# Optimization experiments

Hardware: AMD Instinct MI355X
Metric: run time of the kernel (lower is better)

## Reference

```python
import jax, jax.numpy as jnp
import numpy as np

B = 65536
L, R, D, C = 4, 8, 16, 4
M = D * C          # 64 = d_s2*C
D_S1C = 32         # d_s1*C
OUT = 8


def setup_inputs() -> dict:
    key = jax.random.key(0)
    ks = jax.random.split(key, 16)
    inp = {
        'x': jax.random.uniform(ks[0], (B, 8), dtype=jnp.float32),
        'H': jax.random.normal(ks[1], (B, L, R, D, C), dtype=jnp.float32) * 0.1,
        # VNNILinear / Linear params (not quantized by default -> plain F.linear)
        'W_bit': jax.random.normal(ks[2], (D_S1C, 8), dtype=jnp.float32) * 0.02,
        'b_bit': jnp.zeros((D_S1C,), jnp.float32),
        'W_bridge': jax.random.normal(ks[3], (M, D_S1C), dtype=jnp.float32) * 0.02,
        'W_read': jax.random.normal(ks[4], (OUT, R * M), dtype=jnp.float32) * 0.02,
        'b_read': jnp.zeros((OUT,), jnp.float32),
        # Governor
        'W_sh': jax.random.normal(ks[5], (64, M), dtype=jnp.float32) * 0.02,
        'b_sh': jnp.zeros((64,), jnp.float32),
        'W_eng': jax.random.normal(ks[6], (1, 64), dtype=jnp.float32) * 0.02,
        'b_eng': jnp.zeros((1,), jnp.float32),
        'W_imp': jax.random.normal(ks[7], (1, 64), dtype=jnp.float32) * 0.02,
        'b_imp': jnp.zeros((1,), jnp.float32),
        # surprise heads
        'W_sur': jax.random.normal(ks[8], (1, D_S1C), dtype=jnp.float32) * 0.02,
        'b_sur': jnp.zeros((1,), jnp.float32),
        'W_gate': jax.random.normal(ks[9], (1, D_S1C), dtype=jnp.float32) * 0.02,
        'b_gate': jnp.zeros((1,), jnp.float32),
        # stacked per-slot params
        'decays': jnp.zeros((L, R, M), jnp.float32),
        'halt_w': jax.random.normal(ks[10], (L, R, M), dtype=jnp.float32) * 0.01,
        'halt_b': jnp.zeros((L,), jnp.float32),
    }
    return inp


def reference(x, H, W_bit, b_bit, W_bridge, W_read, b_read, W_sh, b_sh,
              W_eng, b_eng, W_imp, b_imp, W_sur, b_sur, W_gate, b_gate,
              decays, halt_w, halt_b):
    # bit -> s1 latent
    s1 = x @ W_bit.T + b_bit                                   # [B, 32]
    surprise = (jax.nn.sigmoid(s1 @ W_sur.T + b_sur) *
                jax.nn.sigmoid(s1 @ W_gate.T + b_gate))        # [B, 1]
    # bridge to working space
    s2 = jnp.tanh(s1 @ W_bridge.T)                             # [B, 64]
    # governor gates
    hg = jax.nn.relu(s2 @ W_sh.T + b_sh)                       # [B, 64]
    eng = jax.nn.sigmoid(hg @ W_eng.T + b_eng)                 # [B, 1]
    imp = jax.nn.sigmoid(hg @ W_imp.T + b_imp)                 # [B, 1]
    # per-(L,R)-slot halting gate
    halt = jax.nn.sigmoid(jnp.einsum('bm,lrm->blr', s2, halt_w)
                          + halt_b[:, None])                   # [B, L, R]
    gate = halt * (eng * imp)[:, :, None]                      # [B, L, R]
    # gated decay + write into memory slab
    decay_g = jax.nn.sigmoid(decays)                           # [L, R, M]
    Hf = H.reshape(H.shape[0], L, R, M)                        # [B, L, R, M]
    write = (surprise * s2)[:, None, None, :]                  # [B, 1, 1, M]
    H_new = Hf * decay_g[None] + gate[..., None] * write       # [B, L, R, M]
    # read: mean over layers, flatten slots, quantizable readout
    read = H_new.mean(axis=1).reshape(H.shape[0], R * M)       # [B, 512]
    out = read @ W_read.T + b_read                             # [B, 8]
    return out
```

## Files before the change

kernel.cpp:

```cpp
#include <hip/hip_runtime.h>

__device__ __forceinline__ float sigf(float v) {
    return 1.0f / (1.0f + __expf(-v));
}
__device__ __forceinline__ float tanh_fast(float v) {
    return 1.0f - 2.0f / (__expf(2.0f * v) + 1.0f);
}

__global__ __launch_bounds__(256, 1)
void organism_fused(const float* __restrict__ x,
                    const float* __restrict__ H,
                    const float* __restrict__ W_bit,
                    const float* __restrict__ b_bit,
                    const float* __restrict__ W_bridge,
                    const float* __restrict__ W_read,
                    const float* __restrict__ b_read,
                    const float* __restrict__ W_sh,
                    const float* __restrict__ b_sh,
                    const float* __restrict__ W_eng,
                    const float* __restrict__ b_eng,
                    const float* __restrict__ W_imp,
                    const float* __restrict__ b_imp,
                    const float* __restrict__ W_sur,
                    const float* __restrict__ b_sur,
                    const float* __restrict__ W_gate,
                    const float* __restrict__ b_gate,
                    const float* __restrict__ decays,
                    const float* __restrict__ halt_w,
                    const float* __restrict__ halt_b,
                    float* __restrict__ out)
{
    const int b = blockIdx.x * 256 + threadIdx.x;

    float xv[8];
    {
        const float4 x0 = *(const float4*)(x + (size_t)b * 8);
        const float4 x1 = *(const float4*)(x + (size_t)b * 8 + 4);
        xv[0]=x0.x; xv[1]=x0.y; xv[2]=x0.z; xv[3]=x0.w;
        xv[4]=x1.x; xv[5]=x1.y; xv[6]=x1.z; xv[7]=x1.w;
    }

    float s1[32];
#pragma unroll
    for (int i = 0; i < 32; ++i) {
        float a = b_bit[i];
#pragma unroll
        for (int k = 0; k < 8; ++k) a += W_bit[i*8+k] * xv[k];
        s1[i] = a;
    }

    float sa = b_sur[0], ga = b_gate[0];
#pragma unroll
    for (int i = 0; i < 32; ++i) {
        sa += W_sur[i]  * s1[i];
        ga += W_gate[i] * s1[i];
    }
    const float sur = sigf(sa) * sigf(ga);

    float s2[64];
#pragma unroll
    for (int m = 0; m < 64; ++m) {
        float a = 0.0f;
#pragma unroll
        for (int i = 0; i < 32; ++i) a += W_bridge[m*32+i] * s1[i];
        s2[m] = tanh_fast(a);
    }

    float ea = b_eng[0], ia = b_imp[0];
    for (int n = 0; n < 64; ++n) {
        float a = b_sh[n];
#pragma unroll
        for (int m = 0; m < 64; ++m) a += W_sh[n*64+m] * s2[m];
        a = fmaxf(a, 0.0f);
        ea += W_eng[n] * a;
        ia += W_imp[n] * a;
    }
    const float ei = sigf(ea) * sigf(ia);

    float wv[64];
#pragma unroll
    for (int m = 0; m < 64; ++m) wv[m] = sur * s2[m];

    float out2[8] = {0,0,0,0,0,0,0,0};
    for (int r = 0; r < 8; ++r) {
        float hs = 0.0f;
#pragma unroll
        for (int l = 0; l < 4; ++l) {
            float a = halt_b[l];
#pragma unroll
            for (int m = 0; m < 64; ++m) a += halt_w[(l*8+r)*64+m] * s2[m];
            hs += sigf(a);
        }
        const float gr = 0.25f * ei * hs;
#pragma unroll
        for (int o = 0; o < 8; ++o) {
            float p = 0.0f;
#pragma unroll
            for (int m = 0; m < 64; ++m) p += W_read[o*512 + r*64 + m] * wv[m];
            out2[o] += gr * p;
        }
    }

    const float* __restrict__ Hrow = H + (size_t)b * 2048;
    float acc[8] = {0,0,0,0,0,0,0,0};

    const int wid = blockIdx.x * 4 + (threadIdx.x >> 6);
    const int rot = (wid & 7) << 6;

    float4 hA[4][2], hB[4][2];

    auto loadblk = [&](float4 (&h)[4][2], int ib) {
        const int rmb = ((ib << 3) + rot) & 511;
#pragma unroll
        for (int l = 0; l < 4; ++l) {
            h[l][0] = *(const float4*)(Hrow + l*512 + rmb);
            h[l][1] = *(const float4*)(Hrow + l*512 + rmb + 4);
        }
    };
    auto compute = [&](const float4 (&h)[4][2], int ib) {
        const int rmb = ((ib << 3) + rot) & 511;
        float s[8] = {0,0,0,0,0,0,0,0};
#pragma unroll
        for (int l = 0; l < 4; ++l) {
#pragma unroll
            for (int q = 0; q < 2; ++q) {
                const float4 d = *(const float4*)(decays + l*512 + rmb + q*4);
                const float4 hh = h[l][q];
                s[q*4+0] += sigf(d.x) * hh.x;
                s[q*4+1] += sigf(d.y) * hh.y;
                s[q*4+2] += sigf(d.z) * hh.z;
                s[q*4+3] += sigf(d.w) * hh.w;
            }
        }
#pragma unroll
        for (int c = 0; c < 8; ++c) s[c] *= 0.25f;
#pragma unroll
        for (int o = 0; o < 8; ++o) {
#pragma unroll
            for (int q = 0; q < 2; ++q) {
                const float4 wr = *(const float4*)(W_read + o*512 + rmb + q*4);
                acc[o] += wr.x*s[q*4+0] + wr.y*s[q*4+1]
                        + wr.z*s[q*4+2] + wr.w*s[q*4+3];
            }
        }
    };

    loadblk(hA, 0);
#pragma unroll 1
    for (int p = 0; p < 32; ++p) {
        loadblk(hB, 2*p + 1);
        compute(hA, 2*p);
        if (p + 1 < 32) loadblk(hA, 2*p + 2);
        compute(hB, 2*p + 1);
    }

    float4 r0, r1;
    r0.x = acc[0] + out2[0] + b_read[0];
    r0.y = acc[1] + out2[1] + b_read[1];
    r0.z = acc[2] + out2[2] + b_read[2];
    r0.w = acc[3] + out2[3] + b_read[3];
    r1.x = acc[4] + out2[4] + b_read[4];
    r1.y = acc[5] + out2[5] + b_read[5];
    r1.z = acc[6] + out2[6] + b_read[6];
    r1.w = acc[7] + out2[7] + b_read[7];
    *(float4*)(out + (size_t)b * 8)     = r0;
    *(float4*)(out + (size_t)b * 8 + 4) = r1;
}

extern "C" void kernel_launch(void* const* d_in, const int* in_sizes, int n_in,
                              void* d_out, int out_size, void* d_ws, size_t ws_size,
                              hipStream_t stream) {
    (void)n_in; (void)d_ws; (void)ws_size; (void)out_size;
    const float* x        = (const float*)d_in[0];
    const float* H        = (const float*)d_in[1];
    const float* W_bit    = (const float*)d_in[2];
    const float* b_bit    = (const float*)d_in[3];
    const float* W_bridge = (const float*)d_in[4];
    const float* W_read   = (const float*)d_in[5];
    const float* b_read   = (const float*)d_in[6];
    const float* W_sh     = (const float*)d_in[7];
    const float* b_sh     = (const float*)d_in[8];
    const float* W_eng    = (const float*)d_in[9];
    const float* b_eng    = (const float*)d_in[10];
    const float* W_imp    = (const float*)d_in[11];
    const float* b_imp    = (const float*)d_in[12];
    const float* W_sur    = (const float*)d_in[13];
    const float* b_sur    = (const float*)d_in[14];
    const float* W_gate   = (const float*)d_in[15];
    const float* b_gate   = (const float*)d_in[16];
    const float* decays   = (const float*)d_in[17];
    const float* halt_w   = (const float*)d_in[18];
    const float* halt_b   = (const float*)d_in[19];
    float* out = (float*)d_out;

    const int B = in_sizes[1] / 2048;
    dim3 grid(B / 256), block(256);
    hipLaunchKernelGGL(organism_fused, grid, block, 0, stream,
                       x, H, W_bit, b_bit, W_bridge, W_read, b_read,
                       W_sh, b_sh, W_eng, b_eng, W_imp, b_imp,
                       W_sur, b_sur, W_gate, b_gate, decays, halt_w, halt_b,
                       out);
}
```

Measured before the change: 975.8 us.

## Precompute decay sigmoids and stage H through an LDS transpose for coalesced loads

A small prep kernel computes 0.25*sigmoid(decays) once into workspace. This removes the per-row recomputation of 2048 sigmoids in every thread. The main kernel now runs one wavefront per block. That wave loads the H rows of its 64 batch rows cooperatively with coalesced float4 loads and transposes them through a double-buffered, padded LDS tile, prefetching the next chunk into registers. The cost is about 35KB of LDS per single-wave block, which limits occupancy. The code also relies on wave-lockstep LDS ordering instead of explicit barriers.

```diff
diff --git a/kernel.cpp b/kernel.cpp
--- a/kernel.cpp
+++ b/kernel.cpp
@@ -7,35 +7,53 @@
     return 1.0f - 2.0f / (__expf(2.0f * v) + 1.0f);
 }
 
-__global__ __launch_bounds__(256, 1)
-void organism_fused(const float* __restrict__ x,
-                    const float* __restrict__ H,
-                    const float* __restrict__ W_bit,
-                    const float* __restrict__ b_bit,
-                    const float* __restrict__ W_bridge,
-                    const float* __restrict__ W_read,
-                    const float* __restrict__ b_read,
-                    const float* __restrict__ W_sh,
-                    const float* __restrict__ b_sh,
-                    const float* __restrict__ W_eng,
-                    const float* __restrict__ b_eng,
-                    const float* __restrict__ W_imp,
-                    const float* __restrict__ b_imp,
-                    const float* __restrict__ W_sur,
-                    const float* __restrict__ b_sur,
-                    const float* __restrict__ W_gate,
-                    const float* __restrict__ b_gate,
-                    const float* __restrict__ decays,
-                    const float* __restrict__ halt_w,
-                    const float* __restrict__ halt_b,
-                    float* __restrict__ out)
+__global__ void organism_prep(const float* __restrict__ decays,
+                              float* __restrict__ sigd4) {
+    const int i = blockIdx.x * 256 + threadIdx.x;
+    if (i < 2048) sigd4[i] = 0.25f * sigf(decays[i]);
+}
+
+__global__ __launch_bounds__(64)
+void organism_main(const float* __restrict__ x,
+                   const float* __restrict__ H,
+                   const float* __restrict__ W_bit,
+                   const float* __restrict__ b_bit,
+                   const float* __restrict__ W_bridge,
+                   const float* __restrict__ W_read,
+                   const float* __restrict__ b_read,
+                   const float* __restrict__ W_sh,
+                   const float* __restrict__ b_sh,
+                   const float* __restrict__ W_eng,
+                   const float* __restrict__ b_eng,
+                   const float* __restrict__ W_imp,
+                   const float* __restrict__ b_imp,
+                   const float* __restrict__ W_sur,
+                   const float* __restrict__ b_sur,
+                   const float* __restrict__ W_gate,
+                   const float* __restrict__ b_gate,
+                   const float* __restrict__ halt_w,
+                   const float* __restrict__ halt_b,
+                   const float* __restrict__ sigd4,
+                   float* __restrict__ out)
 {
-    const int b = blockIdx.x * 256 + threadIdx.x;
+    const int t   = threadIdx.x;
+    const int row = blockIdx.x * 64 + t;
+    const int lr  = t >> 4;
+    const int lj  = t & 15;
+
+    __shared__ float tile[2][64 * 68];
+
+    const float* __restrict__ Hblk = H + (size_t)blockIdx.x * 64 * 2048;
+
+    float4 pf[16];
+#pragma unroll
+    for (int i = 0; i < 16; ++i)
+        pf[i] = *(const float4*)(Hblk + (size_t)(4 * i + lr) * 2048 + lj * 4);
 
     float xv[8];
     {
-        const float4 x0 = *(const float4*)(x + (size_t)b * 8);
-        const float4 x1 = *(const float4*)(x + (size_t)b * 8 + 4);
+        const float4 x0 = *(const float4*)(x + (size_t)row * 8);
+        const float4 x1 = *(const float4*)(x + (size_t)row * 8 + 4);
         xv[0]=x0.x; xv[1]=x0.y; xv[2]=x0.z; xv[3]=x0.w;
         xv[4]=x1.x; xv[5]=x1.y; xv[6]=x1.z; xv[7]=x1.w;
     }
@@ -101,57 +119,60 @@
         }
     }
 
-    const float* __restrict__ Hrow = H + (size_t)b * 2048;
     float acc[8] = {0,0,0,0,0,0,0,0};
-
-    const int wid = blockIdx.x * 4 + (threadIdx.x >> 6);
-    const int rot = (wid & 7) << 6;
-
-    float4 hA[4][2], hB[4][2];
-
-    auto loadblk = [&](float4 (&h)[4][2], int ib) {
-        const int rmb = ((ib << 3) + rot) & 511;
+    float g[64];
+    int buf = 0;
+
+    auto store_tile = [&](int b) {
+#pragma unroll
+        for (int i = 0; i < 16; ++i)
+            *(float4*)(&tile[b][(4 * i + lr) * 68 + lj * 4]) = pf[i];
+    };
+    auto prefetch = [&](int c, int l) {
+#pragma unroll
+        for (int i = 0; i < 16; ++i)
+            pf[i] = *(const float4*)(Hblk + (size_t)(4 * i + lr) * 2048
+                                     + l * 512 + c * 64 + lj * 4);
+    };
+
+#pragma unroll 1
+    for (int c = 0; c < 8; ++c) {
 #pragma unroll
         for (int l = 0; l < 4; ++l) {
-            h[l][0] = *(const float4*)(Hrow + l*512 + rmb);
-            h[l][1] = *(const float4*)(Hrow + l*512 + rmb + 4);
-        }
-    };
-    auto compute = [&](const float4 (&h)[4][2], int ib) {
-        const int rmb = ((ib << 3) + rot) & 511;
-        float s[8] = {0,0,0,0,0,0,0,0};
-#pragma unroll
-        for (int l = 0; l < 4; ++l) {
-#pragma unroll
-            for (int q = 0; q < 2; ++q) {
-                const float4 d = *(const float4*)(decays + l*512 + rmb + q*4);
-                const float4 hh = h[l][q];
-                s[q*4+0] += sigf(d.x) * hh.x;
-                s[q*4+1] += sigf(d.y) * hh.y;
-                s[q*4+2] += sigf(d.z) * hh.z;
-                s[q*4+3] += sigf(d.w) * hh.w;
+            store_tile(buf);
+            if (l < 3)           prefetch(c, l + 1);
+            else if (c < 7)      prefetch(c + 1, 0);
+            const float* __restrict__ tr = &tile[buf][t * 68];
+            const float* __restrict__ sd = sigd4 + l * 512 + c * 64;
+            if (l == 0) {
+#pragma unroll
+                for (int j = 0; j < 64; j += 4) {
+                    const float4 h = *(const float4*)(tr + j);
+                    g[j]   = sd[j]   * h.x;
+                    g[j+1] = sd[j+1] * h.y;
+                    g[j+2] = sd[j+2] * h.z;
+                    g[j+3] = sd[j+3] * h.w;
+                }
+            } else {
+#pragma unroll
+                for (int j = 0; j < 64; j += 4) {
+                    const float4 h = *(const float4*)(tr + j);
+                    g[j]   += sd[j]   * h.x;
+                    g[j+1] += sd[j+1] * h.y;
+                    g[j+2] += sd[j+2] * h.z;
+                    g[j+3] += sd[j+3] * h.w;
+                }
             }
-        }
-#pragma unroll
-        for (int c = 0; c < 8; ++c) s[c] *= 0.25f;
+            buf ^= 1;
+        }
 #pragma unroll
         for (int o = 0; o < 8; ++o) {
-#pragma unroll
-            for (int q = 0; q < 2; ++q) {
-                const float4 wr = *(const float4*)(W_read + o*512 + rmb + q*4);
-                acc[o] += wr.x*s[q*4+0] + wr.y*s[q*4+1]
-                        + wr.z*s[q*4+2] + wr.w*s[q*4+3];
-            }
-        }
-    };
-
-    loadblk(hA, 0);
-#pragma unroll 1
-    for (int p = 0; p < 32; ++p) {
-        loadblk(hB, 2*p + 1);
-        compute(hA, 2*p);
-        if (p + 1 < 32) loadblk(hA, 2*p + 2);
-        compute(hB, 2*p + 1);
+            const float* __restrict__ wr = W_read + o * 512 + c * 64;
+            float p = 0.0f;
+#pragma unroll
+            for (int j = 0; j < 64; ++j) p += wr[j] * g[j];
+            acc[o] += p;
+        }
     }
 
     float4 r0, r1;
@@ -163,14 +184,14 @@
     r1.y = acc[5] + out2[5] + b_read[5];
     r1.z = acc[6] + out2[6] + b_read[6];
     r1.w = acc[7] + out2[7] + b_read[7];
-    *(float4*)(out + (size_t)b * 8)     = r0;
-    *(float4*)(out + (size_t)b * 8 + 4) = r1;
+    *(float4*)(out + (size_t)row * 8)     = r0;
+    *(float4*)(out + (size_t)row * 8 + 4) = r1;
 }
 
 extern "C" void kernel_launch(void* const* d_in, const int* in_sizes, int n_in,
                               void* d_out, int out_size, void* d_ws, size_t ws_size,
                               hipStream_t stream) {
-    (void)n_in; (void)d_ws; (void)ws_size; (void)out_size;
+    (void)n_in; (void)ws_size; (void)out_size;
     const float* x        = (const float*)d_in[0];
     const float* H        = (const float*)d_in[1];
     const float* W_bit    = (const float*)d_in[2];
@@ -191,13 +212,16 @@
     const float* decays   = (const float*)d_in[17];
     const float* halt_w   = (const float*)d_in[18];
     const float* halt_b   = (const float*)d_in[19];
-    float* out = (float*)d_out;
+    float* out   = (float*)d_out;
+    float* sigd4 = (float*)d_ws;
 
     const int B = in_sizes[1] / 2048;
-    dim3 grid(B / 256), block(256);
-    hipLaunchKernelGGL(organism_fused, grid, block, 0, stream,
+
+    hipLaunchKernelGGL(organism_prep, dim3(8), dim3(256), 0, stream,
+                       decays, sigd4);
+    hipLaunchKernelGGL(organism_main, dim3(B / 64), dim3(64), 0, stream,
                        x, H, W_bit, b_bit, W_bridge, W_read, b_read,
                        W_sh, b_sh, W_eng, b_eng, W_imp, b_imp,
-                       W_sur, b_sur, W_gate, b_gate, decays, halt_w, halt_b,
-                       out);
-}
+                       W_sur, b_sur, W_gate, b_gate, halt_w, halt_b,
+                       sigd4, out);
+}
```

Result: slower. 1.422 ms (+45.7%).

## Stream each H row cooperatively across a wavefront with coalesced loads

Applied to the files above, without the earlier changes.

Before, each thread walked its own 8 KB H row, so a wave's lanes touched addresses 8 KB apart on every load. Now one 64-lane wave handles 32 batch rows and reads one H row per iteration with fully coalesced float4 loads, prefetching the next row. Each lane keeps its column slice of sigmoid(decays) and W_read in registers, and the per-row dot products are reduced across the wave with xor shuffles. The small per-row MLP is computed per lane and held until that row's output is written. This trades cross-lane shuffle work, duplicated MLP work in the upper half-wave, and one wasted prefetch for much better memory coalescing.

```diff
diff --git a/kernel.cpp b/kernel.cpp
--- a/kernel.cpp
+++ b/kernel.cpp
@@ -7,164 +7,182 @@
     return 1.0f - 2.0f / (__expf(2.0f * v) + 1.0f);
 }
 
-__global__ __launch_bounds__(256, 1)
-void organism_fused(const float* __restrict__ x,
-                    const float* __restrict__ H,
-                    const float* __restrict__ W_bit,
-                    const float* __restrict__ b_bit,
-                    const float* __restrict__ W_bridge,
-                    const float* __restrict__ W_read,
-                    const float* __restrict__ b_read,
-                    const float* __restrict__ W_sh,
-                    const float* __restrict__ b_sh,
-                    const float* __restrict__ W_eng,
-                    const float* __restrict__ b_eng,
-                    const float* __restrict__ W_imp,
-                    const float* __restrict__ b_imp,
-                    const float* __restrict__ W_sur,
-                    const float* __restrict__ b_sur,
-                    const float* __restrict__ W_gate,
-                    const float* __restrict__ b_gate,
-                    const float* __restrict__ decays,
-                    const float* __restrict__ halt_w,
-                    const float* __restrict__ halt_b,
-                    float* __restrict__ out)
+__global__ __launch_bounds__(64)
+void organism_main(const float* __restrict__ x,
+                   const float* __restrict__ H,
+                   const float* __restrict__ W_bit,
+                   const float* __restrict__ b_bit,
+                   const float* __restrict__ W_bridge,
+                   const float* __restrict__ W_read,
+                   const float* __restrict__ b_read,
+                   const float* __restrict__ W_sh,
+                   const float* __restrict__ b_sh,
+                   const float* __restrict__ W_eng,
+                   const float* __restrict__ b_eng,
+                   const float* __restrict__ W_imp,
+                   const float* __restrict__ b_imp,
+                   const float* __restrict__ W_sur,
+                   const float* __restrict__ b_sur,
+                   const float* __restrict__ W_gate,
+                   const float* __restrict__ b_gate,
+                   const float* __restrict__ decays,
+                   const float* __restrict__ halt_w,
+                   const float* __restrict__ halt_b,
+                   float* __restrict__ out)
 {
-    const int b = blockIdx.x * 256 + threadIdx.x;
-
-    float xv[8];
+    const int lane = threadIdx.x;
+    const int r0   = blockIdx.x * 32;
+    const int arow = r0 + (lane & 31);
+
+    const float* __restrict__ Hl = H + (size_t)r0 * 2048 + lane * 4;
+    float4 h[8];
+#pragma unroll
+    for (int it = 0; it < 8; ++it)
+        h[it] = *(const float4*)(Hl + it * 256);
+
+    float o2[8];
     {
-        const float4 x0 = *(const float4*)(x + (size_t)b * 8);
-        const float4 x1 = *(const float4*)(x + (size_t)b * 8 + 4);
+        float xv[8];
+        const float4 x0 = *(const float4*)(x + (size_t)arow * 8);
+        const float4 x1 = *(const float4*)(x + (size_t)arow * 8 + 4);
         xv[0]=x0.x; xv[1]=x0.y; xv[2]=x0.z; xv[3]=x0.w;
         xv[4]=x1.x; xv[5]=x1.y; xv[6]=x1.z; xv[7]=x1.w;
+
+        float s1[32];
+#pragma unroll
+        for (int i = 0; i < 32; ++i) {
+            float a = b_bit[i];
+#pragma unroll
+            for (int k = 0; k < 8; ++k) a += W_bit[i*8+k] * xv[k];
+            s1[i] = a;
+        }
+
+        float sa = b_sur[0], ga = b_gate[0];
+#pragma unroll
+        for (int i = 0; i < 32; ++i) {
+            sa += W_sur[i]  * s1[i];
+            ga += W_gate[i] * s1[i];
+        }
+        const float sur = sigf(sa) * sigf(ga);
+
+        float s2[64];
+#pragma unroll
+        for (int m = 0; m < 64; ++m) {
+            float a = 0.0f;
+#pragma unroll
+            for (int i = 0; i < 32; ++i) a += W_bridge[m*32+i] * s1[i];
+            s2[m] = tanh_fast(a);
+        }
+
+        float ea = b_eng[0], ia = b_imp[0];
+        for (int n = 0; n < 64; ++n) {
+            float a = b_sh[n];
+#pragma unroll
+            for (int m = 0; m < 64; ++m) a += W_sh[n*64+m] * s2[m];
+            a = fmaxf(a, 0.0f);
+            ea += W_eng[n] * a;
+            ia += W_imp[n] * a;
+        }
+        const float ei = sigf(ea) * sigf(ia);
+
+        float wv[64];
+#pragma unroll
+        for (int m = 0; m < 64; ++m) wv[m] = sur * s2[m];
+
+#pragma unroll
+        for (int o = 0; o < 8; ++o) o2[o] = b_read[o];
+        for (int r = 0; r < 8; ++r) {
+            float hs = 0.0f;
+#pragma unroll
+            for (int l = 0; l < 4; ++l) {
+                float a = halt_b[l];
+#pragma unroll
+                for (int m = 0; m < 64; ++m) a += halt_w[(l*8+r)*64+m] * s2[m];
+                hs += sigf(a);
+            }
+            const float gr = 0.25f * ei * hs;
+#pragma unroll
+            for (int o = 0; o < 8; ++o) {
+                float p = 0.0f;
+#pragma unroll
+                for (int m = 0; m < 64; ++m) p += W_read[o*512 + r*64 + m] * wv[m];
+                o2[o] += gr * p;
+            }
+        }
     }
 
-    float s1[32];
-#pragma unroll
-    for (int i = 0; i < 32; ++i) {
-        float a = b_bit[i];
-#pragma unroll
-        for (int k = 0; k < 8; ++k) a += W_bit[i*8+k] * xv[k];
-        s1[i] = a;
+    float sd[4][8];
+#pragma unroll
+    for (int l = 0; l < 4; ++l)
+#pragma unroll
+        for (int hf = 0; hf < 2; ++hf) {
+            const float4 d = *(const float4*)(decays + l*512 + hf*256 + lane*4);
+            sd[l][hf*4+0] = 0.25f * sigf(d.x);
+            sd[l][hf*4+1] = 0.25f * sigf(d.y);
+            sd[l][hf*4+2] = 0.25f * sigf(d.z);
+            sd[l][hf*4+3] = 0.25f * sigf(d.w);
+        }
+    float wrv[8][8];
+#pragma unroll
+    for (int o = 0; o < 8; ++o)
+#pragma unroll
+        for (int hf = 0; hf < 2; ++hf) {
+            const float4 w = *(const float4*)(W_read + o*512 + hf*256 + lane*4);
+            wrv[o][hf*4+0] = w.x;
+            wrv[o][hf*4+1] = w.y;
+            wrv[o][hf*4+2] = w.z;
+            wrv[o][hf*4+3] = w.w;
+        }
+
+#pragma unroll 1
+    for (int rr = 0; rr < 32; ++rr) {
+        float g[8];
+#pragma unroll
+        for (int hf = 0; hf < 2; ++hf) {
+            g[hf*4+0] = sd[0][hf*4+0]*h[hf].x   + sd[1][hf*4+0]*h[2+hf].x
+                      + sd[2][hf*4+0]*h[4+hf].x + sd[3][hf*4+0]*h[6+hf].x;
+            g[hf*4+1] = sd[0][hf*4+1]*h[hf].y   + sd[1][hf*4+1]*h[2+hf].y
+                      + sd[2][hf*4+1]*h[4+hf].y + sd[3][hf*4+1]*h[6+hf].y;
+            g[hf*4+2] = sd[0][hf*4+2]*h[hf].z   + sd[1][hf*4+2]*h[2+hf].z
+                      + sd[2][hf*4+2]*h[4+hf].z + sd[3][hf*4+2]*h[6+hf].z;
+            g[hf*4+3] = sd[0][hf*4+3]*h[hf].w   + sd[1][hf*4+3]*h[2+hf].w
+                      + sd[2][hf*4+3]*h[4+hf].w + sd[3][hf*4+3]*h[6+hf].w;
+        }
+
+        {
+            const int nrr = (rr + 1) & 31;
+            const float* __restrict__ nb = H + (size_t)(r0 + nrr) * 2048 + lane * 4;
+#pragma unroll
+            for (int it = 0; it < 8; ++it)
+                h[it] = *(const float4*)(nb + it * 256);
+        }
+
+        float acc[8];
+#pragma unroll
+        for (int o = 0; o < 8; ++o) {
+            float a = 0.0f;
+#pragma unroll
+            for (int s = 0; s < 8; ++s) a += wrv[o][s] * g[s];
+            acc[o] = a;
+        }
+
+#pragma unroll
+        for (int m = 1; m <= 32; m <<= 1) {
+#pragma unroll
+            for (int o = 0; o < 8; ++o)
+                acc[o] += __shfl_xor(acc[o], m, 64);
+        }
+
+        if (lane == rr) {
+            float4 a0, a1;
+            a0.x = acc[0] + o2[0]; a0.y = acc[1] + o2[1];
+            a0.z = acc[2] + o2[2]; a0.w = acc[3] + o2[3];
+            a1.x = acc[4] + o2[4]; a1.y = acc[5] + o2[5];
+            a1.z = acc[6] + o2[6]; a1.w = acc[7] + o2[7];
+            *(float4*)(out + (size_t)(r0 + rr) * 8)     = a0;
+            *(float4*)(out + (size_t)(r0 + rr) * 8 + 4) = a1;
+        }
     }
-
-    float sa = b_sur[0], ga = b_gate[0];
-#pragma unroll
-    for (int i = 0; i < 32; ++i) {
-        sa += W_sur[i]  * s1[i];
-        ga += W_gate[i] * s1[i];
-    }
-    const float sur = sigf(sa) * sigf(ga);
-
-    float s2[64];
-#pragma unroll
-    for (int m = 0; m < 64; ++m) {
-        float a = 0.0f;
-#pragma unroll
-        for (int i = 0; i < 32; ++i) a += W_bridge[m*32+i] * s1[i];
-        s2[m] = tanh_fast(a);
-    }
-
-    float ea = b_eng[0], ia = b_imp[0];
-    for (int n = 0; n < 64; ++n) {
-        float a = b_sh[n];
-#pragma unroll
-        for (int m = 0; m < 64; ++m) a += W_sh[n*64+m] * s2[m];
-        a = fmaxf(a, 0.0f);
-        ea += W_eng[n] * a;
-        ia += W_imp[n] * a;
-    }
-    const float ei = sigf(ea) * sigf(ia);
-
-    float wv[64];
-#pragma unroll
-    for (int m = 0; m < 64; ++m) wv[m] = sur * s2[m];
-
-    float out2[8] = {0,0,0,0,0,0,0,0};
-    for (int r = 0; r < 8; ++r) {
-        float hs = 0.0f;
-#pragma unroll
-        for (int l = 0; l < 4; ++l) {
-            float a = halt_b[l];
-#pragma unroll
-            for (int m = 0; m < 64; ++m) a += halt_w[(l*8+r)*64+m] * s2[m];
-            hs += sigf(a);
-        }
-        const float gr = 0.25f * ei * hs;
-#pragma unroll
-        for (int o = 0; o < 8; ++o) {
-            float p = 0.0f;
-#pragma unroll
-            for (int m = 0; m < 64; ++m) p += W_read[o*512 + r*64 + m] * wv[m];
-            out2[o] += gr * p;
-        }
-    }
-
-    const float* __restrict__ Hrow = H + (size_t)b * 2048;
-    float acc[8] = {0,0,0,0,0,0,0,0};
-
-    const int wid = blockIdx.x * 4 + (threadIdx.x >> 6);
-    const int rot = (wid & 7) << 6;
-
-    float4 hA[4][2], hB[4][2];
-
-    auto loadblk = [&](float4 (&h)[4][2], int ib) {
-        const int rmb = ((ib << 3) + rot) & 511;
-#pragma unroll
-        for (int l = 0; l < 4; ++l) {
-            h[l][0] = *(const float4*)(Hrow + l*512 + rmb);
-            h[l][1] = *(const float4*)(Hrow + l*512 + rmb + 4);
-        }
-    };
-    auto compute = [&](const float4 (&h)[4][2], int ib) {
-        const int rmb = ((ib << 3) + rot) & 511;
-        float s[8] = {0,0,0,0,0,0,0,0};
-#pragma unroll
-        for (int l = 0; l < 4; ++l) {
-#pragma unroll
-            for (int q = 0; q < 2; ++q) {
-                const float4 d = *(const float4*)(decays + l*512 + rmb + q*4);
-                const float4 hh = h[l][q];
-                s[q*4+0] += sigf(d.x) * hh.x;
-                s[q*4+1] += sigf(d.y) * hh.y;
-                s[q*4+2] += sigf(d.z) * hh.z;
-                s[q*4+3] += sigf(d.w) * hh.w;
-            }
-        }
-#pragma unroll
-        for (int c = 0; c < 8; ++c) s[c] *= 0.25f;
-#pragma unroll
-        for (int o = 0; o < 8; ++o) {
-#pragma unroll
-            for (int q = 0; q < 2; ++q) {
-                const float4 wr = *(const float4*)(W_read + o*512 + rmb + q*4);
-                acc[o] += wr.x*s[q*4+0] + wr.y*s[q*4+1]
-                        + wr.z*s[q*4+2] + wr.w*s[q*4+3];
-            }
-        }
-    };
-
-    loadblk(hA, 0);
-#pragma unroll 1
-    for (int p = 0; p < 32; ++p) {
-        loadblk(hB, 2*p + 1);
-        compute(hA, 2*p);
-        if (p + 1 < 32) loadblk(hA, 2*p + 2);
-        compute(hB, 2*p + 1);
-    }
-
-    float4 r0, r1;
-    r0.x = acc[0] + out2[0] + b_read[0];
-    r0.y = acc[1] + out2[1] + b_read[1];
-    r0.z = acc[2] + out2[2] + b_read[2];
-    r0.w = acc[3] + out2[3] + b_read[3];
-    r1.x = acc[4] + out2[4] + b_read[4];
-    r1.y = acc[5] + out2[5] + b_read[5];
-    r1.z = acc[6] + out2[6] + b_read[6];
-    r1.w = acc[7] + out2[7] + b_read[7];
-    *(float4*)(out + (size_t)b * 8)     = r0;
-    *(float4*)(out + (size_t)b * 8 + 4) = r1;
 }
 
 extern "C" void kernel_launch(void* const* d_in, const int* in_sizes, int n_in,
@@ -194,8 +212,7 @@
     float* out = (float*)d_out;
 
     const int B = in_sizes[1] / 2048;
-    dim3 grid(B / 256), block(256);
-    hipLaunchKernelGGL(organism_fused, grid, block, 0, stream,
+    hipLaunchKernelGGL(organism_main, dim3(B / 32), dim3(64), 0, stream,
                        x, H, W_bit, b_bit, W_bridge, W_read, b_read,
                        W_sh, b_sh, W_eng, b_eng, W_imp, b_imp,
                        W_sur, b_sur, W_gate, b_gate, decays, halt_w, halt_b,
```

Result: faster. 889.1 us (-8.9%).
